# Kernel optimization log

Hardware: AMD Instinct MI355X
Metric: run time of the kernel (lower is better)

## Reference

```python
import jax, jax.numpy as jnp
import numpy as np

EMBED_DIM = 1024
B, QL, KL = 4, 2048, 2048

def setup_inputs() -> dict:
    key = jax.random.key(0)
    k1, k2, k3, k4 = jax.random.split(key, 4)
    hidden_states = jax.random.normal(k1, (B, QL, EMBED_DIM), dtype=jnp.float32)
    decoder_hidden_states = jax.random.normal(k2, (B, KL, EMBED_DIM), dtype=jnp.float32)
    # Linear weights stored as [in, out] (torch stores [out, in]; math identical via x @ W)
    Wq = jax.random.normal(k3, (EMBED_DIM, EMBED_DIM), dtype=jnp.float32) * (1.0 / np.sqrt(EMBED_DIM))
    Wkv = jax.random.normal(k4, (EMBED_DIM, 2 * EMBED_DIM), dtype=jnp.float32) * (1.0 / np.sqrt(EMBED_DIM))
    return {"hidden_states": hidden_states, "decoder_hidden_states": decoder_hidden_states,
            "Wq": Wq, "Wkv": Wkv}

def reference(hidden_states, decoder_hidden_states, Wq, Wkv):
    d = Wq.shape[0]
    scale = 1.0 / np.sqrt(d)
    query = hidden_states @ Wq                      # [B, QL, D]
    kv = decoder_hidden_states @ Wkv                # [B, KL, 2D]
    key, value = jnp.split(kv, 2, axis=-1)          # each [B, KL, D]
    scores = jnp.einsum('bqd,bkd->bqk', query, key) * scale  # [B, QL, KL]
    w = jax.nn.softmax(scores, axis=-1)
    return jnp.einsum('bqk,bkd->bqd', w, value)     # [B, QL, D]
```

## Files before the change

kernel.cpp:

```cpp
#include <hip/hip_runtime.h>
#include <stdint.h>


typedef __bf16 bf16_t;
typedef __bf16 bf16x8 __attribute__((ext_vector_type(8)));
typedef __bf16 bf16x4 __attribute__((ext_vector_type(4)));
typedef float  f32x4  __attribute__((ext_vector_type(4)));

#define MFMA_BF16(A, B, C) __builtin_amdgcn_mfma_f32_16x16x32_bf16((A), (B), (C), 0, 0, 0)
#define ATTN_SHIFT 16.0f

__device__ __forceinline__ void async_copy16(const void* g, void* l) {
  __builtin_amdgcn_global_load_lds(
      (const __attribute__((address_space(1))) uint32_t*)g,
      (__attribute__((address_space(3))) uint32_t*)l, 16, 0, 0);
}

#define PH_PRE()                                             \
  do {                                                       \
    __builtin_amdgcn_sched_barrier(0);                       \
    __builtin_amdgcn_s_barrier();                            \
    asm volatile("s_waitcnt lgkmcnt(0)" ::: "memory");       \
    __builtin_amdgcn_sched_barrier(0);                       \
    __builtin_amdgcn_s_setprio(1);                           \
  } while (0)
#define PH_POST()                                            \
  do {                                                       \
    __builtin_amdgcn_s_setprio(0);                           \
    __builtin_amdgcn_sched_barrier(0);                       \
    __builtin_amdgcn_s_barrier();                            \
  } while (0)

__global__ void prep_kernel(const float* __restrict__ a, const float* __restrict__ b,
                            bf16_t* __restrict__ ab, bf16_t* __restrict__ bb,
                            float* __restrict__ rowsum, int n) {
  int gtid = blockIdx.x * blockDim.x + threadIdx.x;
  if (gtid < 8192) rowsum[gtid] = 0.f;
  int idx = gtid * 4;
  int stride = gridDim.x * blockDim.x * 4;
  for (int i = idx; i < n; i += stride) {
    float4 v = *(const float4*)(a + i);
    float4 w = *(const float4*)(b + i);
    bf16x4 o, p;
    o[0] = (bf16_t)v.x; o[1] = (bf16_t)v.y; o[2] = (bf16_t)v.z; o[3] = (bf16_t)v.w;
    p[0] = (bf16_t)w.x; p[1] = (bf16_t)w.y; p[2] = (bf16_t)w.z; p[3] = (bf16_t)w.w;
    *(bf16x4*)(ab + i) = o;
    *(bf16x4*)(bb + i) = p;
  }
}

__global__ void transpose_both_kernel(const float* __restrict__ Wq, const float* __restrict__ Wkv,
                                      bf16_t* __restrict__ WqT, bf16_t* __restrict__ WkvT) {
  __shared__ float tile[32][33];
  int bx = blockIdx.x;
  const float* src; bf16_t* dst; int R, C; float scale;
  int cb;
  if (bx < 32) { src = Wq;  dst = WqT;  R = 1024; C = 1024; scale = 0.03125f; cb = bx; }
  else         { src = Wkv; dst = WkvT; R = 1024; C = 2048; scale = 1.0f;     cb = bx - 32; }
  int c0 = cb * 32, r0 = blockIdx.y * 32;
  int tx = threadIdx.x, ty = threadIdx.y;
#pragma unroll
  for (int i = 0; i < 4; ++i) {
    int r = ty + i * 8;
    tile[r][tx] = src[(size_t)(r0 + r) * C + c0 + tx] * scale;
  }
  __syncthreads();
#pragma unroll
  for (int i = 0; i < 4; ++i) {
    int c = ty + i * 8;
    dst[(size_t)(c0 + c) * R + r0 + tx] = (bf16_t)tile[tx][c];
  }
}

template <int BN, int EPI>
__global__ __launch_bounds__(512, 2) void gemm8(
    const bf16_t* __restrict__ A, int lda, size_t sA,
    const bf16_t* __restrict__ Bt, int ldb, size_t sB,
    void* __restrict__ Cv, int ldc, size_t sC,
    void* __restrict__ Cv2, int nb, int bpb, int K, float* __restrict__ rowsum) {
  constexpr int ABYTES = 256 * 64 * 2;
  constexpr int BBYTES = BN * 64 * 2;
  constexpr int NCF = BN / 64;
  __shared__ char smem[2 * ABYTES + 2 * BBYTES];

  const int bx0 = blockIdx.x;
  const int q8 = gridDim.x >> 3;
  const int swz = (bx0 & 7) * q8 + (bx0 >> 3);
  const int bz = swz / bpb;
  const int rr = swz % bpb;
  const int m0 = (rr / nb) << 8;
  const int n0 = (rr % nb) * BN;

  const bf16_t* Ab = A + (size_t)bz * sA;
  const bf16_t* Bb = Bt + (size_t)bz * sB;
  const int tid = threadIdx.x, w = tid >> 6, l = tid & 63;
  const int l15 = l & 15, l4 = l >> 4;
  const int wr = w >> 2, wc = w & 3;
  const int NT = K >> 6;

  const int lrow = l >> 3;
  const int gcol = ((l & 7) ^ lrow) << 3;
  const bf16_t* PA = Ab + (size_t)(m0 + 8 * w + lrow) * lda + gcol;
  const bf16_t* PB = Bb + (size_t)(n0 + 8 * w + lrow) * ldb + gcol;

  const int sw16 = (l15 & 7) << 4;
  const int aoff0 = (wr * 128 + l15) * 128;
  const int boff0 = (wc * (BN / 4) + l15) * 128;

  f32x4 acc[8][NCF] = {};
  bf16x8 af[4][2], bfr[NCF][2];

  auto stageA = [&](int t, int h) {
    if (t >= NT) return;
    const bf16_t* s = PA + (size_t)(h * 128) * lda + (t << 6);
    char* d = smem + (t & 1) * ABYTES + h * 16384 + w * 1024;
    async_copy16(s, d);
    async_copy16(s + (size_t)64 * lda, d + 8192);
  };
  auto stageB = [&](int t, int h) {
    if (t >= NT) return;
    const bf16_t* s = PB + (size_t)(h * (BN / 2)) * ldb + (t << 6);
    char* d = smem + 2 * ABYTES + (t & 1) * BBYTES + h * (BBYTES / 2) + w * 1024;
    async_copy16(s, d);
    if constexpr (BN == 256) async_copy16(s + (size_t)64 * ldb, d + 8192);
  };

  stageB(0, 0); stageA(0, 0); stageA(0, 1); stageB(0, 1);
  __builtin_amdgcn_sched_barrier(0);
  stageB(1, 0); stageA(1, 0);
  __builtin_amdgcn_sched_barrier(0);
  if constexpr (BN == 256) asm volatile("s_waitcnt vmcnt(4)" ::: "memory");
  else                     asm volatile("s_waitcnt vmcnt(3)" ::: "memory");
  __builtin_amdgcn_s_barrier();

  for (int t = 0; t < NT; ++t) {
    const int cur = t & 1;
    const char* Ac = smem + cur * ABYTES;
    const char* Bc = smem + 2 * ABYTES + cur * BBYTES;
#pragma unroll
    for (int rf = 0; rf < 4; ++rf)
#pragma unroll
      for (int kh = 0; kh < 2; ++kh)
        af[rf][kh] = *(const bf16x8*)(Ac + aoff0 + rf * 2048 + ((((kh * 4 + l4) << 4)) ^ sw16));
#pragma unroll
    for (int cf = 0; cf < NCF / 2; ++cf)
#pragma unroll
      for (int kh = 0; kh < 2; ++kh)
        bfr[cf][kh] = *(const bf16x8*)(Bc + boff0 + cf * 2048 + ((((kh * 4 + l4) << 4)) ^ sw16));
    stageA(t + 1, 1);
    PH_PRE();
#pragma unroll
    for (int rf = 0; rf < 4; ++rf)
#pragma unroll
      for (int cf = 0; cf < NCF / 2; ++cf) {
        acc[rf][cf] = MFMA_BF16(af[rf][0], bfr[cf][0], acc[rf][cf]);
        acc[rf][cf] = MFMA_BF16(af[rf][1], bfr[cf][1], acc[rf][cf]);
      }
    PH_POST();
#pragma unroll
    for (int cf = NCF / 2; cf < NCF; ++cf)
#pragma unroll
      for (int kh = 0; kh < 2; ++kh)
        bfr[cf][kh] = *(const bf16x8*)(Bc + boff0 + cf * 2048 + ((((kh * 4 + l4) << 4)) ^ sw16));
    stageB(t + 1, 1);
    PH_PRE();
#pragma unroll
    for (int rf = 0; rf < 4; ++rf)
#pragma unroll
      for (int cf = NCF / 2; cf < NCF; ++cf) {
        acc[rf][cf] = MFMA_BF16(af[rf][0], bfr[cf][0], acc[rf][cf]);
        acc[rf][cf] = MFMA_BF16(af[rf][1], bfr[cf][1], acc[rf][cf]);
      }
    PH_POST();
#pragma unroll
    for (int rf = 0; rf < 4; ++rf)
#pragma unroll
      for (int kh = 0; kh < 2; ++kh)
        af[rf][kh] = *(const bf16x8*)(Ac + aoff0 + 8192 + rf * 2048 + ((((kh * 4 + l4) << 4)) ^ sw16));
    stageB(t + 2, 0);
    PH_PRE();
#pragma unroll
    for (int rf = 0; rf < 4; ++rf)
#pragma unroll
      for (int cf = 0; cf < NCF / 2; ++cf) {
        acc[4 + rf][cf] = MFMA_BF16(af[rf][0], bfr[cf][0], acc[4 + rf][cf]);
        acc[4 + rf][cf] = MFMA_BF16(af[rf][1], bfr[cf][1], acc[4 + rf][cf]);
      }
    PH_POST();
    stageA(t + 2, 0);
    PH_PRE();
#pragma unroll
    for (int rf = 0; rf < 4; ++rf)
#pragma unroll
      for (int cf = NCF / 2; cf < NCF; ++cf) {
        acc[4 + rf][cf] = MFMA_BF16(af[rf][0], bfr[cf][0], acc[4 + rf][cf]);
        acc[4 + rf][cf] = MFMA_BF16(af[rf][1], bfr[cf][1], acc[4 + rf][cf]);
      }
    __builtin_amdgcn_s_setprio(0);
    __builtin_amdgcn_sched_barrier(0);
    if (t < NT - 2) {
      if constexpr (BN == 256) asm volatile("s_waitcnt vmcnt(4)" ::: "memory");
      else                     asm volatile("s_waitcnt vmcnt(3)" ::: "memory");
    } else {
      asm volatile("s_waitcnt vmcnt(0)" ::: "memory");
    }
    __builtin_amdgcn_s_barrier();
  }

  __syncthreads();

  if constexpr (EPI == 0) {
    bf16_t* Cb = (bf16_t*)Cv + (size_t)bz * sC;
#pragma unroll
    for (int arf = 0; arf < 8; ++arf)
#pragma unroll
      for (int cf = 0; cf < NCF; ++cf) {
        int grow = m0 + wr * 128 + arf * 16 + l4 * 4;
        int gc = n0 + wc * (BN / 4) + cf * 16 + l15;
#pragma unroll
        for (int r = 0; r < 4; ++r)
          Cb[(size_t)(grow + r) * ldc + gc] = (bf16_t)acc[arf][cf][r];
      }
  } else if constexpr (EPI == 1) {
    bf16_t* Cb = (bf16_t*)Cv + (size_t)bz * sC;
    float* rsh = (float*)smem;
    if (tid < 256) rsh[tid] = 0.f;
    __syncthreads();
#pragma unroll
    for (int arf = 0; arf < 8; ++arf)
#pragma unroll
      for (int r = 0; r < 4; ++r) {
        int lr = wr * 128 + arf * 16 + l4 * 4 + r;
        float s = 0.f;
#pragma unroll
        for (int cf = 0; cf < NCF; ++cf) {
          float p = __expf(acc[arf][cf][r] - ATTN_SHIFT);
          bf16_t pb = (bf16_t)p;
          Cb[(size_t)(m0 + lr) * ldc + n0 + wc * (BN / 4) + cf * 16 + l15] = pb;
          s += (float)pb;
        }
        s += __shfl_xor(s, 1); s += __shfl_xor(s, 2);
        s += __shfl_xor(s, 4); s += __shfl_xor(s, 8);
        if (l15 == 0) atomicAdd(&rsh[lr], s);
      }
    __syncthreads();
    if (tid < 256) atomicAdd(&rowsum[(size_t)bz * 2048 + m0 + tid], rsh[tid]);
  } else if constexpr (EPI == 2) {
    float* rsh = (float*)smem;
    if (tid < 256) rsh[tid] = rowsum[(size_t)bz * 2048 + m0 + tid];
    __syncthreads();
    float* Cb = (float*)Cv + (size_t)bz * sC;
#pragma unroll
    for (int arf = 0; arf < 8; ++arf)
#pragma unroll
      for (int r = 0; r < 4; ++r) {
        float inv = 1.0f / rsh[wr * 128 + arf * 16 + l4 * 4 + r];
        int grow = m0 + wr * 128 + arf * 16 + l4 * 4 + r;
#pragma unroll
        for (int cf = 0; cf < NCF; ++cf)
          Cb[(size_t)grow * ldc + n0 + wc * (BN / 4) + cf * 16 + l15] = acc[arf][cf][r] * inv;
      }
  } else {
    if (n0 < 1024) {
      bf16_t* Cb = (bf16_t*)Cv;
#pragma unroll
      for (int arf = 0; arf < 8; ++arf)
#pragma unroll
        for (int cf = 0; cf < NCF; ++cf) {
          int grow = m0 + wr * 128 + arf * 16 + l4 * 4;
          int gc = n0 + wc * (BN / 4) + cf * 16 + l15;
#pragma unroll
          for (int r = 0; r < 4; ++r)
            Cb[(size_t)(grow + r) * ldc + gc] = (bf16_t)acc[arf][cf][r];
        }
    } else {
      bf16_t* VTb = (bf16_t*)Cv2;
#pragma unroll
      for (int arf = 0; arf < 8; ++arf)
#pragma unroll
        for (int cf = 0; cf < NCF; ++cf) {
          int grow0 = m0 + wr * 128 + arf * 16 + l4 * 4;
          int b = grow0 >> 11, kl = grow0 & 2047;
          int d = (n0 - 1024) + wc * (BN / 4) + cf * 16 + l15;
          bf16x4 v;
#pragma unroll
          for (int r = 0; r < 4; ++r) v[r] = (bf16_t)acc[arf][cf][r];
          *(bf16x4*)(VTb + (size_t)b * (1024 * 2048) + (size_t)d * 2048 + kl) = v;
        }
    }
  }
}

extern "C" void kernel_launch(void* const* d_in, const int* in_sizes, int n_in,
                              void* d_out, int out_size, void* d_ws, size_t ws_size,
                              hipStream_t stream) {
  const float* hs  = (const float*)d_in[0];
  const float* dhs = (const float*)d_in[1];
  const float* Wq  = (const float*)d_in[2];
  const float* Wkv = (const float*)d_in[3];
  float* out = (float*)d_out;

  const size_t M1 = 1024 * 1024;
  bf16_t* WqT  = (bf16_t*)d_ws;
  bf16_t* WkvT = WqT + M1;
  bf16_t* AB   = WkvT + 2 * M1;
  bf16_t* dhsb = AB;
  bf16_t* hsb  = AB + 8 * M1;
  bf16_t* P    = AB;
  bf16_t* Kb   = AB + 16 * M1;
  bf16_t* VTb  = Kb + 8 * M1;
  bf16_t* Qb   = VTb + 8 * M1;
  float* rowsum = (float*)(Qb + 8 * M1);

  prep_kernel<<<2048, 256, 0, stream>>>(dhs, hs, dhsb, hsb, rowsum, 8192 * 1024);
  transpose_both_kernel<<<dim3(96, 32), dim3(32, 8), 0, stream>>>(Wq, Wkv, WqT, WkvT);

  gemm8<256, 4><<<256, 512, 0, stream>>>(
      dhsb, 1024, 0, WkvT, 1024, 0, Kb, 1024, 0, VTb, 8, 256, 1024, nullptr);
  gemm8<128, 0><<<256, 512, 0, stream>>>(
      hsb, 1024, 0, WqT, 1024, 0, Qb, 1024, 0, nullptr, 8, 256, 1024, nullptr);
  gemm8<256, 1><<<256, 512, 0, stream>>>(
      Qb, 1024, (size_t)2048 * 1024, Kb, 1024, (size_t)2048 * 1024,
      P, 2048, (size_t)2048 * 2048, nullptr, 8, 64, 1024, rowsum);
  gemm8<128, 2><<<256, 512, 0, stream>>>(
      P, 2048, (size_t)2048 * 2048, VTb, 2048, (size_t)1024 * 2048,
      out, 1024, (size_t)2048 * 1024, nullptr, 8, 64, 2048, rowsum);
}
```

Measured before the change: 167.3 us.

## Merge prep and transpose kernels; coarsen GEMM main loop to two phases

Folds the activation fp32→bf16 conversion and the weight transpose kernels into one launch, using separate block ranges, which removes one kernel launch and its gap. In the GEMM main loop, all B fragments are now loaded up front and the four barrier-delimited MFMA phases become two larger ones, halving the barriers and priority toggles per K-step. The initial staging order is also changed to issue the A tiles first. The trade-offs are higher register pressure from holding every B fragment at once and less overlap between LDS reads and MFMA work.

```diff
diff --git a/kernel.cpp b/kernel.cpp
--- a/kernel.cpp
+++ b/kernel.cpp
@@ -33,42 +33,43 @@
 
 __global__ void prep_kernel(const float* __restrict__ a, const float* __restrict__ b,
                             bf16_t* __restrict__ ab, bf16_t* __restrict__ bb,
-                            float* __restrict__ rowsum, int n) {
-  int gtid = blockIdx.x * blockDim.x + threadIdx.x;
-  if (gtid < 8192) rowsum[gtid] = 0.f;
-  int idx = gtid * 4;
-  int stride = gridDim.x * blockDim.x * 4;
-  for (int i = idx; i < n; i += stride) {
-    float4 v = *(const float4*)(a + i);
-    float4 w = *(const float4*)(b + i);
-    bf16x4 o, p;
-    o[0] = (bf16_t)v.x; o[1] = (bf16_t)v.y; o[2] = (bf16_t)v.z; o[3] = (bf16_t)v.w;
-    p[0] = (bf16_t)w.x; p[1] = (bf16_t)w.y; p[2] = (bf16_t)w.z; p[3] = (bf16_t)w.w;
-    *(bf16x4*)(ab + i) = o;
-    *(bf16x4*)(bb + i) = p;
-  }
-}
-
-__global__ void transpose_both_kernel(const float* __restrict__ Wq, const float* __restrict__ Wkv,
-                                      bf16_t* __restrict__ WqT, bf16_t* __restrict__ WkvT) {
+                            float* __restrict__ rowsum,
+                            const float* __restrict__ Wq, const float* __restrict__ Wkv,
+                            bf16_t* __restrict__ WqT, bf16_t* __restrict__ WkvT) {
   __shared__ float tile[32][33];
-  int bx = blockIdx.x;
-  const float* src; bf16_t* dst; int R, C; float scale;
-  int cb;
-  if (bx < 32) { src = Wq;  dst = WqT;  R = 1024; C = 1024; scale = 0.03125f; cb = bx; }
-  else         { src = Wkv; dst = WkvT; R = 1024; C = 2048; scale = 1.0f;     cb = bx - 32; }
-  int c0 = cb * 32, r0 = blockIdx.y * 32;
-  int tx = threadIdx.x, ty = threadIdx.y;
-#pragma unroll
-  for (int i = 0; i < 4; ++i) {
-    int r = ty + i * 8;
-    tile[r][tx] = src[(size_t)(r0 + r) * C + c0 + tx] * scale;
-  }
-  __syncthreads();
-#pragma unroll
-  for (int i = 0; i < 4; ++i) {
-    int c = ty + i * 8;
-    dst[(size_t)(c0 + c) * R + r0 + tx] = (bf16_t)tile[tx][c];
+  const int bx = blockIdx.x, tid = threadIdx.x;
+  if (bx < 2048) {
+    int gtid = bx * 256 + tid;
+    if (gtid < 8192) rowsum[gtid] = 0.f;
+    const int n = 8 * 1024 * 1024, stride = 2048 * 256 * 4;
+    for (int i = gtid * 4; i < n; i += stride) {
+      float4 v = *(const float4*)(a + i);
+      float4 w = *(const float4*)(b + i);
+      bf16x4 o, p;
+      o[0] = (bf16_t)v.x; o[1] = (bf16_t)v.y; o[2] = (bf16_t)v.z; o[3] = (bf16_t)v.w;
+      p[0] = (bf16_t)w.x; p[1] = (bf16_t)w.y; p[2] = (bf16_t)w.z; p[3] = (bf16_t)w.w;
+      *(bf16x4*)(ab + i) = o;
+      *(bf16x4*)(bb + i) = p;
+    }
+  } else {
+    int t = bx - 2048;
+    int r0 = (t / 96) * 32, cb = t % 96;
+    const float* src; bf16_t* dst; int R, C; float scale;
+    if (cb < 32) { src = Wq;  dst = WqT;  R = 1024; C = 1024; scale = 0.03125f; }
+    else         { src = Wkv; dst = WkvT; R = 1024; C = 2048; scale = 1.0f; cb -= 32; }
+    int c0 = cb * 32;
+    int tx = tid & 31, ty = tid >> 5;
+#pragma unroll
+    for (int i = 0; i < 4; ++i) {
+      int r = ty + i * 8;
+      tile[r][tx] = src[(size_t)(r0 + r) * C + c0 + tx] * scale;
+    }
+    __syncthreads();
+#pragma unroll
+    for (int i = 0; i < 4; ++i) {
+      int c = ty + i * 8;
+      dst[(size_t)(c0 + c) * R + r0 + tx] = (bf16_t)tile[tx][c];
+    }
   }
 }
 
@@ -125,7 +126,7 @@
     if constexpr (BN == 256) async_copy16(s + (size_t)64 * ldb, d + 8192);
   };
 
-  stageB(0, 0); stageA(0, 0); stageA(0, 1); stageB(0, 1);
+  stageA(0, 0); stageA(0, 1); stageB(0, 0); stageB(0, 1);
   __builtin_amdgcn_sched_barrier(0);
   stageB(1, 0); stageA(1, 0);
   __builtin_amdgcn_sched_barrier(0);
@@ -143,31 +144,17 @@
       for (int kh = 0; kh < 2; ++kh)
         af[rf][kh] = *(const bf16x8*)(Ac + aoff0 + rf * 2048 + ((((kh * 4 + l4) << 4)) ^ sw16));
 #pragma unroll
-    for (int cf = 0; cf < NCF / 2; ++cf)
+    for (int cf = 0; cf < NCF; ++cf)
 #pragma unroll
       for (int kh = 0; kh < 2; ++kh)
         bfr[cf][kh] = *(const bf16x8*)(Bc + boff0 + cf * 2048 + ((((kh * 4 + l4) << 4)) ^ sw16));
     stageA(t + 1, 1);
-    PH_PRE();
-#pragma unroll
-    for (int rf = 0; rf < 4; ++rf)
-#pragma unroll
-      for (int cf = 0; cf < NCF / 2; ++cf) {
-        acc[rf][cf] = MFMA_BF16(af[rf][0], bfr[cf][0], acc[rf][cf]);
-        acc[rf][cf] = MFMA_BF16(af[rf][1], bfr[cf][1], acc[rf][cf]);
-      }
-    PH_POST();
-#pragma unroll
-    for (int cf = NCF / 2; cf < NCF; ++cf)
-#pragma unroll
-      for (int kh = 0; kh < 2; ++kh)
-        bfr[cf][kh] = *(const bf16x8*)(Bc + boff0 + cf * 2048 + ((((kh * 4 + l4) << 4)) ^ sw16));
     stageB(t + 1, 1);
     PH_PRE();
 #pragma unroll
     for (int rf = 0; rf < 4; ++rf)
 #pragma unroll
-      for (int cf = NCF / 2; cf < NCF; ++cf) {
+      for (int cf = 0; cf < NCF; ++cf) {
         acc[rf][cf] = MFMA_BF16(af[rf][0], bfr[cf][0], acc[rf][cf]);
         acc[rf][cf] = MFMA_BF16(af[rf][1], bfr[cf][1], acc[rf][cf]);
       }
@@ -178,21 +165,12 @@
       for (int kh = 0; kh < 2; ++kh)
         af[rf][kh] = *(const bf16x8*)(Ac + aoff0 + 8192 + rf * 2048 + ((((kh * 4 + l4) << 4)) ^ sw16));
     stageB(t + 2, 0);
-    PH_PRE();
-#pragma unroll
-    for (int rf = 0; rf < 4; ++rf)
-#pragma unroll
-      for (int cf = 0; cf < NCF / 2; ++cf) {
-        acc[4 + rf][cf] = MFMA_BF16(af[rf][0], bfr[cf][0], acc[4 + rf][cf]);
-        acc[4 + rf][cf] = MFMA_BF16(af[rf][1], bfr[cf][1], acc[4 + rf][cf]);
-      }
-    PH_POST();
     stageA(t + 2, 0);
     PH_PRE();
 #pragma unroll
     for (int rf = 0; rf < 4; ++rf)
 #pragma unroll
-      for (int cf = NCF / 2; cf < NCF; ++cf) {
+      for (int cf = 0; cf < NCF; ++cf) {
         acc[4 + rf][cf] = MFMA_BF16(af[rf][0], bfr[cf][0], acc[4 + rf][cf]);
         acc[4 + rf][cf] = MFMA_BF16(af[rf][1], bfr[cf][1], acc[4 + rf][cf]);
       }
@@ -312,8 +290,8 @@
   bf16_t* Qb   = VTb + 8 * M1;
   float* rowsum = (float*)(Qb + 8 * M1);
 
-  prep_kernel<<<2048, 256, 0, stream>>>(dhs, hs, dhsb, hsb, rowsum, 8192 * 1024);
-  transpose_both_kernel<<<dim3(96, 32), dim3(32, 8), 0, stream>>>(Wq, Wkv, WqT, WkvT);
+  prep_kernel<<<2048 + 3072, 256, 0, stream>>>(dhs, hs, dhsb, hsb, rowsum,
+                                               Wq, Wkv, WqT, WkvT);
 
   gemm8<256, 4><<<256, 512, 0, stream>>>(
       dhsb, 1024, 0, WkvT, 1024, 0, Kb, 1024, 0, VTb, 8, 256, 1024, nullptr);
```

New measurement: 160.2 us. 4.2% less time.
